# Optimization experiments

Hardware: AMD Instinct MI355X
Metric: run time of the kernel (lower is better)

The kernel has to match this reference:

```python
import jax, jax.numpy as jnp
import numpy as np

K = 3        # kernel size (square)
PAD = 1
STRIDE = 1


def conv2d(x, w, b, stride=STRIDE, pad=PAD):
    out = jax.lax.conv_general_dilated(
        x, w, (stride, stride), [(pad, pad), (pad, pad)],
        dimension_numbers=('NCHW', 'OIHW', 'NCHW'))
    return out + b[None, :, None, None]


def deform_sample(x, offset, mask):
    """Bilinear sampling at learned offsets (torchvision deform_conv2d v2 semantics).
    x: (B,C,H,W); offset: (B,2*K*K,Ho,Wo) as (dy,dx) pairs per kernel tap;
    mask: (B,K*K,Ho,Wo) already sigmoided. Returns (B,C,K*K,Ho,Wo)."""
    B, C, H, W = x.shape
    KK = mask.shape[1]
    Ho, Wo = offset.shape[2], offset.shape[3]
    off = offset.reshape(B, KK, 2, Ho, Wo)
    dy, dx = off[:, :, 0], off[:, :, 1]                      # (B,KK,Ho,Wo)
    ky, kx = jnp.meshgrid(jnp.arange(K), jnp.arange(K), indexing='ij')
    ky = ky.reshape(-1).astype(x.dtype)                       # (KK,)
    kx = kx.reshape(-1).astype(x.dtype)
    base_y = (jnp.arange(Ho) * STRIDE - PAD).astype(x.dtype)  # (Ho,)
    base_x = (jnp.arange(Wo) * STRIDE - PAD).astype(x.dtype)
    py = base_y[None, None, :, None] + ky[None, :, None, None] + dy
    px = base_x[None, None, None, :] + kx[None, :, None, None] + dx
    y0 = jnp.floor(py)
    x0 = jnp.floor(px)
    wy1 = py - y0; wx1 = px - x0
    wy0 = 1.0 - wy1; wx0 = 1.0 - wx1

    def gather(yi, xi):
        # zero-padded bilinear corner gather -> (B,C,KK,Ho,Wo)
        valid = ((yi >= 0) & (yi < H) & (xi >= 0) & (xi < W)).astype(x.dtype)
        yc = jnp.clip(yi, 0, H - 1).astype(jnp.int32)
        xc = jnp.clip(xi, 0, W - 1).astype(jnp.int32)
        vals = jax.vmap(lambda xb, yb, xib: xb[:, yb, xib])(x, yc, xc)
        return vals * valid[:, None]

    samp = (gather(y0, x0) * (wy0 * wx0)[:, None]
            + gather(y0, x0 + 1.0) * (wy0 * wx1)[:, None]
            + gather(y0 + 1.0, x0) * (wy1 * wx0)[:, None]
            + gather(y0 + 1.0, x0 + 1.0) * (wy1 * wx1)[:, None])
    return samp * mask[:, None]


def setup_inputs() -> dict:
    key = jax.random.key(0)
    k = jax.random.split(key, 8)
    B, Cin, Cout, H, W = 4, 256, 256, 64, 64
    stdv = 1.0 / np.sqrt(Cin * K * K)
    x = jax.random.normal(k[0], (B, Cin, H, W), dtype=jnp.float32)
    weight = jax.random.uniform(k[1], (Cout, Cin, K, K), minval=-stdv, maxval=stdv, dtype=jnp.float32)
    bias = jnp.zeros((Cout,), dtype=jnp.float32)
    # offset/mask convs are zero-init in the original; use small random values
    # so the irregular-sampling path is actually exercised.
    off_w = jax.random.normal(k[2], (2 * K * K, Cin, K, K), dtype=jnp.float32) * 0.01
    off_b = jax.random.normal(k[3], (2 * K * K,), dtype=jnp.float32) * 0.5
    mask_w = jax.random.normal(k[4], (K * K, Cin, K, K), dtype=jnp.float32) * 0.01
    mask_b = jax.random.normal(k[5], (K * K,), dtype=jnp.float32) * 0.1
    return {"x": x, "weight": weight, "bias": bias,
            "off_w": off_w, "off_b": off_b, "mask_w": mask_w, "mask_b": mask_b}


def reference(x, weight, bias, off_w, off_b, mask_w, mask_b):
    offset = conv2d(x, off_w, off_b)                      # (B,2*KK,H,W)
    mask = jax.nn.sigmoid(conv2d(x, mask_w, mask_b))      # (B,KK,H,W)
    samp = deform_sample(x, offset, mask)                 # (B,C,KK,H,W)
    O, C = weight.shape[0], weight.shape[1]
    out = jnp.einsum('bckhw,ock->bohw', samp, weight.reshape(O, C, K * K))
    return out + bias[None, :, None, None]
```

## Files before the change

### kernel.cpp

```cpp
#include <hip/hip_runtime.h>
#include <hip/hip_bf16.h>
#include <string.h>


typedef __attribute__((ext_vector_type(8))) short short8;
typedef __attribute__((ext_vector_type(8))) _Float16 half8;
typedef __attribute__((ext_vector_type(2))) _Float16 half2v;
typedef __attribute__((ext_vector_type(16))) float floatx16;

__device__ __forceinline__ unsigned bfbits(float f) {
    unsigned u;
    __builtin_memcpy(&u, &f, 4);
    return (u + 0x7fffu + ((u >> 16) & 1u)) >> 16;
}
__device__ __forceinline__ unsigned pack_bf16(float lo, float hi) {
    return bfbits(lo) | (bfbits(hi) << 16);
}
__device__ __forceinline__ unsigned pack_f16(float lo, float hi) {
    _Float16 a = (_Float16)lo, b = (_Float16)hi;
    unsigned short ua, ub;
    __builtin_memcpy(&ua, &a, 2);
    __builtin_memcpy(&ub, &b, 2);
    return (unsigned)ua | ((unsigned)ub << 16);
}

__device__ __forceinline__ void gl_lds16(const void* g, void* l) {
    __builtin_amdgcn_global_load_lds(
        (const __attribute__((address_space(1))) unsigned int*)g,
        (__attribute__((address_space(3))) unsigned int*)l,
        16, 0, 0);
}

__global__ __launch_bounds__(256) void xpose_hwc_kernel(
    const float* __restrict__ x, unsigned short* __restrict__ xt)
{
    __shared__ float stage[256 * 65];
    const int bid = blockIdx.x;
    const int b = bid >> 6, y = bid & 63;
    const int tid = threadIdx.x;
    const float* src = x + (size_t)b * 256 * 4096 + y * 64;

#pragma unroll
    for (int i = 0; i < 16; ++i) {
        int idx = i * 256 + tid;
        int c = idx >> 4, xq = idx & 15;
        float4 v = *(const float4*)&src[(size_t)c * 4096 + xq * 4];
        stage[c * 65 + xq * 4 + 0] = v.x;
        stage[c * 65 + xq * 4 + 1] = v.y;
        stage[c * 65 + xq * 4 + 2] = v.z;
        stage[c * 65 + xq * 4 + 3] = v.w;
    }
    __syncthreads();

    unsigned short* dst = xt + (size_t)bid * 16384;
#pragma unroll
    for (int i = 0; i < 32; ++i) {
        int c2 = (tid & 127) * 2;
        int xx = i * 2 + (tid >> 7);
        float f0 = stage[c2 * 65 + xx];
        float f1 = stage[(c2 + 1) * 65 + xx];
        *(unsigned*)&dst[xx * 256 + c2] = pack_f16(f0, f1);
    }
}

__global__ __launch_bounds__(256) void weight_pack_kernel(
    const float* __restrict__ w, const float* __restrict__ off_w,
    const float* __restrict__ mask_w,
    unsigned short* __restrict__ ws_b, unsigned short* __restrict__ ws_a2)
{
    __shared__ float slab[32 * 289];
    const int bid = blockIdx.x;
    const int tid = threadIdx.x;

    if (bid < 64) {
        const int nt = bid >> 3, cb = bid & 7;
        const float* wbase = w + (size_t)nt * 32 * 2304 + cb * 288;
#pragma unroll
        for (int i = 0; i < 9; ++i) {
            int idx = i * 256 + tid;
            int o = idx / 72, f4 = idx % 72;
            float4 v = *(const float4*)&wbase[(size_t)o * 2304 + f4 * 4];
            slab[o * 289 + f4 * 4 + 0] = v.x;
            slab[o * 289 + f4 * 4 + 1] = v.y;
            slab[o * 289 + f4 * 4 + 2] = v.z;
            slab[o * 289 + f4 * 4 + 3] = v.w;
        }
        __syncthreads();
#pragma unroll
        for (int pass = 0; pass < 5; ++pass) {
            int rid = pass * 8 + (tid >> 5);
            if (rid < 36) {
                int kk = rid >> 2, q = rid & 3;
                int no = tid & 31;
                unsigned pk[4];
#pragma unroll
                for (int i = 0; i < 4; ++i) {
                    float f0 = slab[no * 289 + (q * 8 + 2 * i) * 9 + kk];
                    float f1 = slab[no * 289 + (q * 8 + 2 * i + 1) * 9 + kk];
                    pk[i] = pack_f16(f0, f1);
                }
                size_t u = ((size_t)nt * 288 + kk * 32 + cb * 4 + q) * 32 + no;
                *(uint4*)&ws_b[u * 8] = make_uint4(pk[0], pk[1], pk[2], pk[3]);
            }
        }
    } else {
        int e = (bid - 64) * 256 + tid;
        int lan = e & 31;
        int ku = e >> 5;
        int kk = ku >> 5;
        int c0 = (ku & 31) * 8;
        int o = lan;
        float f[8];
#pragma unroll
        for (int j = 0; j < 8; ++j) {
            int c = c0 + j;
            float v = 0.f;
            if (o < 18)      v = off_w[((size_t)o * 256 + c) * 9 + kk];
            else if (o < 27) v = mask_w[((size_t)(o - 18) * 256 + c) * 9 + kk];
            f[j] = v;
        }
        unsigned pk[4];
#pragma unroll
        for (int i = 0; i < 4; ++i) pk[i] = pack_f16(f[2 * i], f[2 * i + 1]);
        *(uint4*)&ws_a2[(size_t)e * 8] = make_uint4(pk[0], pk[1], pk[2], pk[3]);
    }
}

__global__ __launch_bounds__(512) void offmask_mfma_kernel(
    const unsigned short* __restrict__ xt, const unsigned short* __restrict__ ws_a2,
    const float* __restrict__ off_b, const float* __restrict__ mask_b,
    float* __restrict__ ws_off)
{
    __shared__ uint4 stage[3 * 66 * 32];
    const int bid = blockIdx.x;
    const int row = (bid & 7) * 32 + (bid >> 3);
    const int b = row >> 6, ho = row & 63;
    const int tid = threadIdx.x;
    const int l = tid & 63;
    const int w = tid >> 6;
    const int lan = l & 31, h = l >> 5;
    const int ntile = w >> 2, kq = w & 3;

    const char* xtb = (const char*)xt + (size_t)b * 64 * 32768;
    for (int r = 0; r < 3; ++r) {
        int y = ho - 1 + r;
        uint4* rowbase = &stage[r * 66 * 32];
        if (y >= 0 && y < 64) {
            const char* src = xtb + (size_t)y * 32768;
#pragma unroll
            for (int i = 0; i < 4; ++i) {
                int g0 = 32 + (w * 4 + i) * 64;
                int g = g0 + l;
                int p01 = g >> 5, j = g & 31;
                int kul = j ^ (p01 & 7);
                gl_lds16(src + ((size_t)(p01 - 1) * 32 + kul) * 16,
                         rowbase + g0);
            }
            if (tid < 64) {
                int g = (tid < 32) ? tid : (2080 + (tid - 32));
                rowbase[g] = make_uint4(0, 0, 0, 0);
            }
        } else {
            for (int g = tid; g < 2112; g += 512)
                rowbase[g] = make_uint4(0, 0, 0, 0);
        }
    }
    __syncthreads();

    floatx16 acc;
#pragma unroll
    for (int r = 0; r < 16; ++r) acc[r] = 0.f;

    const uint4* a4 = (const uint4*)ws_a2;
    const int n = ntile * 32 + lan;
#pragma unroll
    for (int ky = 0; ky < 3; ++ky) {
#pragma unroll
        for (int kx = 0; kx < 3; ++kx) {
            int kk = ky * 3 + kx;
            int p01 = n + kx;
#pragma unroll
            for (int s4 = 0; s4 < 4; ++s4) {
                int s = kq * 4 + s4;
                int kul = s * 2 + h;
                uint4 ua = a4[(size_t)(kk * 32 + kul) * 32 + lan];
                uint4 ub = stage[(ky * 66 + p01) * 32 + (kul ^ (p01 & 7))];
                half8 a, bb;
                __builtin_memcpy(&a, &ua, 16);
                __builtin_memcpy(&bb, &ub, 16);
                acc = __builtin_amdgcn_mfma_f32_32x32x16_f16(a, bb, acc, 0, 0, 0);
            }
        }
    }
    __syncthreads();

    float* red = (float*)stage;
#pragma unroll
    for (int r = 0; r < 16; ++r) red[(w * 64 + l) * 16 + r] = acc[r];
    __syncthreads();
    for (int idx = tid; idx < 27 * 64; idx += 512) {
        int oc = idx >> 6, wo = idx & 63;
        int nt2 = wo >> 5, nn = wo & 31;
        int h2 = (oc >> 2) & 1;
        int r = (oc & 3) | ((oc >> 3) << 2);
        int lane2 = nn + 32 * h2;
        float s = 0.f;
#pragma unroll
        for (int kq2 = 0; kq2 < 4; ++kq2)
            s += red[((nt2 * 4 + kq2) * 64 + lane2) * 16 + r];
        float v;
        if (oc < 18) {
            v = s + off_b[oc];
        } else {
            float t = s + mask_b[oc - 18];
            v = 1.f / (1.f + expf(-t));
        }
        ws_off[(size_t)row * 1728 + idx] = v;
    }
}

__global__ __launch_bounds__(512, 2) void deform_gemm_kernel(
    const unsigned short* __restrict__ xt, const float* __restrict__ ws_off,
    const unsigned short* __restrict__ ws_b, const float* __restrict__ bias,
    float* __restrict__ out)
{
    __shared__ uint4 paramw[576];
    __shared__ ushort4 paramo[576];
    __shared__ float biasl[256];
    __shared__ uint4 tile[2][2048];

    const int bid = blockIdx.x;
    const int row = (bid & 7) * 32 + (bid >> 3);
    const int b = row >> 6, ho = row & 63;
    const int tid = threadIdx.x;
    const int l = tid & 63;
    const int wid = tid >> 6;
    const int lan = l & 31;
    const int h = l >> 5;

    if (tid < 256) biasl[tid] = bias[tid];

    {
        const float* ob = ws_off + (size_t)row * 1728;
        for (int it = tid; it < 576; it += 512) {
            int kk = it >> 6, p = it & 63;
            float dy = ob[(2 * kk) * 64 + p];
            float dx = ob[(2 * kk + 1) * 64 + p];
            float mk = ob[(18 + kk) * 64 + p];
            int ky = kk / 3, kx = kk - ky * 3;
            float py = (float)(ho - 1 + ky) + dy;
            float px = (float)(p - 1 + kx) + dx;
            float y0f = floorf(py), x0f = floorf(px);
            float wy1 = py - y0f, wx1 = px - x0f;
            float wy0 = 1.f - wy1, wx0 = 1.f - wx1;
            int y0 = (int)y0f, xi0 = (int)x0f;
            int y1 = y0 + 1, xi1 = xi0 + 1;
            float vy0 = (y0 >= 0 && y0 < 64) ? 1.f : 0.f;
            float vy1 = (y1 >= 0 && y1 < 64) ? 1.f : 0.f;
            float vx0 = (xi0 >= 0 && xi0 < 64) ? 1.f : 0.f;
            float vx1 = (xi1 >= 0 && xi1 < 64) ? 1.f : 0.f;
            float wr0 = wy0 * vy0 * mk, wr1 = wy1 * vy1 * mk;
            float wa = wx0 * vx0, wb2 = wx1 * vx1;
            int yc0 = min(max(y0, 0), 63), yc1 = min(max(y1, 0), 63);
            int xc0 = min(max(xi0, 0), 63), xc1 = min(max(xi1, 0), 63);
            float a00 = wr0 * wa, a01 = wr0 * wb2;
            float a10 = wr1 * wa, a11 = wr1 * wb2;
            paramw[it] = make_uint4(pack_f16(a00, a00), pack_f16(a01, a01),
                                    pack_f16(a10, a10), pack_f16(a11, a11));
            paramo[it] = make_ushort4((unsigned short)(yc0 * 64 + xc0),
                                      (unsigned short)(yc0 * 64 + xc1),
                                      (unsigned short)(yc1 * 64 + xc0),
                                      (unsigned short)(yc1 * 64 + xc1));
        }
    }
    __syncthreads();

    const char* xb16 = (const char*)xt + ((size_t)b << 21);
    const uint4* wb4 = (const uint4*)ws_b;

    floatx16 acc0, acc1;
#pragma unroll
    for (int r = 0; r < 16; ++r) { acc0[r] = 0.f; acc1[r] = 0.f; }

    uint4 gA[2][4], gB[2][4];
    uint4 wvA[2], wvB[2];
    uint4 uaA[8], uaB[8];

    auto issue_half = [&](int kk, int i0, uint4 (&g)[2][4], uint4 (&wv)[2]) {
#pragma unroll
        for (int i = 0; i < 2; ++i) {
            int p = wid * 8 + 2 * (i0 + i) + h;
            int e = kk * 64 + p;
            wv[i] = paramw[e];
            ushort4 uo = paramo[e];
            __builtin_memcpy(&g[i][0], xb16 + ((int)uo.x << 9) + (lan << 4), 16);
            __builtin_memcpy(&g[i][1], xb16 + ((int)uo.y << 9) + (lan << 4), 16);
            __builtin_memcpy(&g[i][2], xb16 + ((int)uo.z << 9) + (lan << 4), 16);
            __builtin_memcpy(&g[i][3], xb16 + ((int)uo.w << 9) + (lan << 4), 16);
        }
    };

    auto pack_half = [&](int buf, int i0, uint4 (&g)[2][4], uint4 (&wv)[2]) {
        char* tb = (char*)&tile[buf][0];
#pragma unroll
        for (int i = 0; i < 2; ++i) {
            int p = wid * 8 + 2 * (i0 + i) + h;
            half2v c00[4], c01[4], c10[4], c11[4], w00, w01, w10, w11;
            __builtin_memcpy(&c00, &g[i][0], 16);
            __builtin_memcpy(&c01, &g[i][1], 16);
            __builtin_memcpy(&c10, &g[i][2], 16);
            __builtin_memcpy(&c11, &g[i][3], 16);
            __builtin_memcpy(&w00, &wv[i].x, 4);
            __builtin_memcpy(&w01, &wv[i].y, 4);
            __builtin_memcpy(&w10, &wv[i].z, 4);
            __builtin_memcpy(&w11, &wv[i].w, 4);
            uint4 outv;
            unsigned* op = (unsigned*)&outv;
#pragma unroll
            for (int j = 0; j < 4; ++j) {
                half2v r = c00[j] * w00;
                r = c01[j] * w01 + r;
                r = c10[j] * w10 + r;
                r = c11[j] * w11 + r;
                __builtin_memcpy(&op[j], &r, 4);
            }
            __builtin_memcpy(tb + lan * 1024 + ((p << 4) ^ (lan << 4)), &outv, 16);
        }
    };

    issue_half(0, 0, gA, wvA);
    pack_half(0, 0, gA, wvA);
    issue_half(0, 2, gB, wvB);
    pack_half(0, 2, gB, wvB);
#pragma unroll
    for (int ks = 0; ks < 8; ++ks) {
        int kul = ks * 2 + h;
        uaA[ks] = wb4[((size_t)wid * 288 + 0 * 32 + kul) * 32 + lan];
    }
    __syncthreads();

    for (int kk = 0; kk < 9; ++kk) {
        const int buf = kk & 1, nbuf = (kk + 1) & 1;

#pragma unroll
        for (int ks = 0; ks < 8; ++ks) {
            int kul = (ks + 8) * 2 + h;
            uaB[ks] = wb4[((size_t)wid * 288 + kk * 32 + kul) * 32 + lan];
        }
        if (kk < 8) issue_half(kk + 1, 0, gA, wvA);
        __builtin_amdgcn_sched_barrier(0);

        {
            const char* tb = (const char*)&tile[buf][0];
#pragma unroll
            for (int ks = 0; ks < 8; ++ks) {
                int kul = ks * 2 + h;
                uint4 ub0, ub1;
                __builtin_memcpy(&ub0, tb + kul * 1024 + ((lan << 4) ^ (kul << 4)), 16);
                __builtin_memcpy(&ub1, tb + kul * 1024 + (((32 + lan) << 4) ^ (kul << 4)), 16);
                half8 a, b0, b1;
                __builtin_memcpy(&a, &uaA[ks], 16);
                __builtin_memcpy(&b0, &ub0, 16);
                __builtin_memcpy(&b1, &ub1, 16);
                acc0 = __builtin_amdgcn_mfma_f32_32x32x16_f16(a, b0, acc0, 0, 0, 0);
                acc1 = __builtin_amdgcn_mfma_f32_32x32x16_f16(a, b1, acc1, 0, 0, 0);
            }
        }
        __builtin_amdgcn_sched_barrier(0);

        if (kk < 8) {
#pragma unroll
            for (int ks = 0; ks < 8; ++ks) {
                int kul = ks * 2 + h;
                uaA[ks] = wb4[((size_t)wid * 288 + (kk + 1) * 32 + kul) * 32 + lan];
            }
            pack_half(nbuf, 0, gA, wvA);
            issue_half(kk + 1, 2, gB, wvB);
        }
        __builtin_amdgcn_sched_barrier(0);

        {
            const char* tb = (const char*)&tile[buf][0];
#pragma unroll
            for (int ks = 0; ks < 8; ++ks) {
                int kul = (ks + 8) * 2 + h;
                uint4 ub0, ub1;
                __builtin_memcpy(&ub0, tb + kul * 1024 + ((lan << 4) ^ (kul << 4)), 16);
                __builtin_memcpy(&ub1, tb + kul * 1024 + (((32 + lan) << 4) ^ (kul << 4)), 16);
                half8 a, b0, b1;
                __builtin_memcpy(&a, &uaB[ks], 16);
                __builtin_memcpy(&b0, &ub0, 16);
                __builtin_memcpy(&b1, &ub1, 16);
                acc0 = __builtin_amdgcn_mfma_f32_32x32x16_f16(a, b0, acc0, 0, 0, 0);
                acc1 = __builtin_amdgcn_mfma_f32_32x32x16_f16(a, b1, acc1, 0, 0, 0);
            }
        }
        __builtin_amdgcn_sched_barrier(0);

        if (kk < 8) pack_half(nbuf, 2, gB, wvB);
        __syncthreads();
    }

#pragma unroll
    for (int nt = 0; nt < 2; ++nt) {
#pragma unroll
        for (int r = 0; r < 16; ++r) {
            int o = wid * 32 + (r & 3) + 8 * (r >> 2) + 4 * h;
            int woo = nt * 32 + lan;
            float v = (nt == 0) ? acc0[r] : acc1[r];
            out[(((size_t)b * 256 + o) * 64 + ho) * 64 + woo] = v + biasl[o];
        }
    }
}

extern "C" void kernel_launch(void* const* d_in, const int* in_sizes, int n_in,
                              void* d_out, int out_size, void* d_ws, size_t ws_size,
                              hipStream_t stream) {
    const float* x      = (const float*)d_in[0];
    const float* weight = (const float*)d_in[1];
    const float* bias   = (const float*)d_in[2];
    const float* off_w  = (const float*)d_in[3];
    const float* off_b  = (const float*)d_in[4];
    const float* mask_w = (const float*)d_in[5];
    const float* mask_b = (const float*)d_in[6];
    float* out = (float*)d_out;

    float* ws_off = (float*)d_ws;
    unsigned short* ws_b  = (unsigned short*)((char*)d_ws + 1769472);
    unsigned short* ws_a2 = (unsigned short*)((char*)d_ws + 2949120);
    unsigned short* xt    = (unsigned short*)((char*)d_ws + 3096576);

    hipLaunchKernelGGL(weight_pack_kernel, dim3(100), dim3(256), 0, stream,
                       weight, off_w, mask_w, ws_b, ws_a2);
    hipLaunchKernelGGL(xpose_hwc_kernel, dim3(256), dim3(256), 0, stream,
                       x, xt);
    hipLaunchKernelGGL(offmask_mfma_kernel, dim3(256), dim3(512), 0, stream,
                       xt, ws_a2, off_b, mask_b, ws_off);
    hipLaunchKernelGGL(deform_gemm_kernel, dim3(256), dim3(512), 0, stream,
                       xt, ws_off, ws_b, bias, out);
}
```

Before: 124.0 us.

## Fuse offset/mask conv into deformable GEMM kernel via shared LDS

Merges the offset/mask MFMA convolution kernel into the deformable sampling GEMM kernel. Each block computes its row's offsets and mask into shared memory and then runs the sampling GEMM, reusing one LDS buffer for the staging, reduction and tile regions. This removes one kernel launch and the global round-trip of the offset workspace. In exchange the fused kernel needs a large static LDS allocation (about 100KB plus extras), which may limit occupancy to one block per CU despite the launch bound of 2, and it serializes the two phases within each block.

```diff
diff --git a/kernel.cpp b/kernel.cpp
--- a/kernel.cpp
+++ b/kernel.cpp
@@ -126,108 +126,16 @@
     }
 }
 
-__global__ __launch_bounds__(512) void offmask_mfma_kernel(
-    const unsigned short* __restrict__ xt, const unsigned short* __restrict__ ws_a2,
+__global__ __launch_bounds__(512, 2) void fused_deform_kernel(
+    const unsigned short* __restrict__ xt,
+    const unsigned short* __restrict__ ws_a2,
+    const unsigned short* __restrict__ ws_b,
     const float* __restrict__ off_b, const float* __restrict__ mask_b,
-    float* __restrict__ ws_off)
+    const float* __restrict__ bias, float* __restrict__ out)
 {
-    __shared__ uint4 stage[3 * 66 * 32];
-    const int bid = blockIdx.x;
-    const int row = (bid & 7) * 32 + (bid >> 3);
-    const int b = row >> 6, ho = row & 63;
-    const int tid = threadIdx.x;
-    const int l = tid & 63;
-    const int w = tid >> 6;
-    const int lan = l & 31, h = l >> 5;
-    const int ntile = w >> 2, kq = w & 3;
-
-    const char* xtb = (const char*)xt + (size_t)b * 64 * 32768;
-    for (int r = 0; r < 3; ++r) {
-        int y = ho - 1 + r;
-        uint4* rowbase = &stage[r * 66 * 32];
-        if (y >= 0 && y < 64) {
-            const char* src = xtb + (size_t)y * 32768;
-#pragma unroll
-            for (int i = 0; i < 4; ++i) {
-                int g0 = 32 + (w * 4 + i) * 64;
-                int g = g0 + l;
-                int p01 = g >> 5, j = g & 31;
-                int kul = j ^ (p01 & 7);
-                gl_lds16(src + ((size_t)(p01 - 1) * 32 + kul) * 16,
-                         rowbase + g0);
-            }
-            if (tid < 64) {
-                int g = (tid < 32) ? tid : (2080 + (tid - 32));
-                rowbase[g] = make_uint4(0, 0, 0, 0);
-            }
-        } else {
-            for (int g = tid; g < 2112; g += 512)
-                rowbase[g] = make_uint4(0, 0, 0, 0);
-        }
-    }
-    __syncthreads();
-
-    floatx16 acc;
-#pragma unroll
-    for (int r = 0; r < 16; ++r) acc[r] = 0.f;
-
-    const uint4* a4 = (const uint4*)ws_a2;
-    const int n = ntile * 32 + lan;
-#pragma unroll
-    for (int ky = 0; ky < 3; ++ky) {
-#pragma unroll
-        for (int kx = 0; kx < 3; ++kx) {
-            int kk = ky * 3 + kx;
-            int p01 = n + kx;
-#pragma unroll
-            for (int s4 = 0; s4 < 4; ++s4) {
-                int s = kq * 4 + s4;
-                int kul = s * 2 + h;
-                uint4 ua = a4[(size_t)(kk * 32 + kul) * 32 + lan];
-                uint4 ub = stage[(ky * 66 + p01) * 32 + (kul ^ (p01 & 7))];
-                half8 a, bb;
-                __builtin_memcpy(&a, &ua, 16);
-                __builtin_memcpy(&bb, &ub, 16);
-                acc = __builtin_amdgcn_mfma_f32_32x32x16_f16(a, bb, acc, 0, 0, 0);
-            }
-        }
-    }
-    __syncthreads();
-
-    float* red = (float*)stage;
-#pragma unroll
-    for (int r = 0; r < 16; ++r) red[(w * 64 + l) * 16 + r] = acc[r];
-    __syncthreads();
-    for (int idx = tid; idx < 27 * 64; idx += 512) {
-        int oc = idx >> 6, wo = idx & 63;
-        int nt2 = wo >> 5, nn = wo & 31;
-        int h2 = (oc >> 2) & 1;
-        int r = (oc & 3) | ((oc >> 3) << 2);
-        int lane2 = nn + 32 * h2;
-        float s = 0.f;
-#pragma unroll
-        for (int kq2 = 0; kq2 < 4; ++kq2)
-            s += red[((nt2 * 4 + kq2) * 64 + lane2) * 16 + r];
-        float v;
-        if (oc < 18) {
-            v = s + off_b[oc];
-        } else {
-            float t = s + mask_b[oc - 18];
-            v = 1.f / (1.f + expf(-t));
-        }
-        ws_off[(size_t)row * 1728 + idx] = v;
-    }
-}
-
-__global__ __launch_bounds__(512, 2) void deform_gemm_kernel(
-    const unsigned short* __restrict__ xt, const float* __restrict__ ws_off,
-    const unsigned short* __restrict__ ws_b, const float* __restrict__ bias,
-    float* __restrict__ out)
-{
-    __shared__ uint4 paramw[576];
-    __shared__ ushort4 paramo[576];
+    __shared__ __align__(16) char smem[101376];
+    __shared__ float offrow[1728];
     __shared__ float biasl[256];
-    __shared__ uint4 tile[2][2048];
 
     const int bid = blockIdx.x;
     const int row = (bid & 7) * 32 + (bid >> 3);
@@ -235,18 +143,100 @@
     const int tid = threadIdx.x;
     const int l = tid & 63;
     const int wid = tid >> 6;
-    const int lan = l & 31;
-    const int h = l >> 5;
+    const int lan = l & 31, h = l >> 5;
 
     if (tid < 256) biasl[tid] = bias[tid];
 
     {
-        const float* ob = ws_off + (size_t)row * 1728;
+        uint4* stage = (uint4*)smem;
+        const int ntile = wid >> 2, kq = wid & 3;
+        const char* xtb = (const char*)xt + (size_t)b * 64 * 32768;
+        for (int r = 0; r < 3; ++r) {
+            int y = ho - 1 + r;
+            uint4* rowbase = &stage[r * 66 * 32];
+            if (y >= 0 && y < 64) {
+                const char* src = xtb + (size_t)y * 32768;
+#pragma unroll
+                for (int i = 0; i < 4; ++i) {
+                    int g0 = 32 + (wid * 4 + i) * 64;
+                    int g = g0 + l;
+                    int p01 = g >> 5, j = g & 31;
+                    int kul = j ^ (p01 & 7);
+                    gl_lds16(src + ((size_t)(p01 - 1) * 32 + kul) * 16,
+                             rowbase + g0);
+                }
+                if (tid < 64) {
+                    int g = (tid < 32) ? tid : (2080 + (tid - 32));
+                    rowbase[g] = make_uint4(0, 0, 0, 0);
+                }
+            } else {
+                for (int g = tid; g < 2112; g += 512)
+                    rowbase[g] = make_uint4(0, 0, 0, 0);
+            }
+        }
+        __syncthreads();
+
+        floatx16 acc;
+#pragma unroll
+        for (int r = 0; r < 16; ++r) acc[r] = 0.f;
+
+        const uint4* a4 = (const uint4*)ws_a2;
+        const int n = ntile * 32 + lan;
+#pragma unroll
+        for (int ky = 0; ky < 3; ++ky) {
+#pragma unroll
+            for (int kx = 0; kx < 3; ++kx) {
+                int kk = ky * 3 + kx;
+                int p01 = n + kx;
+#pragma unroll
+                for (int s4 = 0; s4 < 4; ++s4) {
+                    int s = kq * 4 + s4;
+                    int kul = s * 2 + h;
+                    uint4 ua = a4[(size_t)(kk * 32 + kul) * 32 + lan];
+                    uint4 ub = stage[(ky * 66 + p01) * 32 + (kul ^ (p01 & 7))];
+                    half8 a, bb;
+                    __builtin_memcpy(&a, &ua, 16);
+                    __builtin_memcpy(&bb, &ub, 16);
+                    acc = __builtin_amdgcn_mfma_f32_32x32x16_f16(a, bb, acc, 0, 0, 0);
+                }
+            }
+        }
+        __syncthreads();
+
+        float* red = (float*)smem;
+#pragma unroll
+        for (int r = 0; r < 16; ++r) red[(wid * 64 + l) * 16 + r] = acc[r];
+        __syncthreads();
+        for (int idx = tid; idx < 27 * 64; idx += 512) {
+            int oc = idx >> 6, wo = idx & 63;
+            int nt2 = wo >> 5, nn = wo & 31;
+            int h2 = (oc >> 2) & 1;
+            int r = (oc & 3) | ((oc >> 3) << 2);
+            int lane2 = nn + 32 * h2;
+            float s = 0.f;
+#pragma unroll
+            for (int kq2 = 0; kq2 < 4; ++kq2)
+                s += red[((nt2 * 4 + kq2) * 64 + lane2) * 16 + r];
+            float v;
+            if (oc < 18) {
+                v = s + off_b[oc];
+            } else {
+                float t = s + mask_b[oc - 18];
+                v = 1.f / (1.f + expf(-t));
+            }
+            offrow[idx] = v;
+        }
+    }
+    __syncthreads();
+
+    uint4*   paramw = (uint4*)(smem + 65536);
+    ushort4* paramo = (ushort4*)(smem + 65536 + 9216);
+    {
         for (int it = tid; it < 576; it += 512) {
             int kk = it >> 6, p = it & 63;
-            float dy = ob[(2 * kk) * 64 + p];
-            float dx = ob[(2 * kk + 1) * 64 + p];
-            float mk = ob[(18 + kk) * 64 + p];
+            float dy = offrow[(2 * kk) * 64 + p];
+            float dx = offrow[(2 * kk + 1) * 64 + p];
+            float mk = offrow[(18 + kk) * 64 + p];
             int ky = kk / 3, kx = kk - ky * 3;
             float py = (float)(ho - 1 + ky) + dy;
             float px = (float)(p - 1 + kx) + dx;
@@ -301,7 +291,7 @@
     };
 
     auto pack_half = [&](int buf, int i0, uint4 (&g)[2][4], uint4 (&wv)[2]) {
-        char* tb = (char*)&tile[buf][0];
+        char* tb = smem + buf * 32768;
 #pragma unroll
         for (int i = 0; i < 2; ++i) {
             int p = wid * 8 + 2 * (i0 + i) + h;
@@ -351,7 +341,7 @@
         __builtin_amdgcn_sched_barrier(0);
 
         {
-            const char* tb = (const char*)&tile[buf][0];
+            const char* tb = smem + buf * 32768;
 #pragma unroll
             for (int ks = 0; ks < 8; ++ks) {
                 int kul = ks * 2 + h;
@@ -380,7 +370,7 @@
         __builtin_amdgcn_sched_barrier(0);
 
         {
-            const char* tb = (const char*)&tile[buf][0];
+            const char* tb = smem + buf * 32768;
 #pragma unroll
             for (int ks = 0; ks < 8; ++ks) {
                 int kul = (ks + 8) * 2 + h;
@@ -425,17 +415,14 @@
     const float* mask_b = (const float*)d_in[6];
     float* out = (float*)d_out;
 
-    float* ws_off = (float*)d_ws;
-    unsigned short* ws_b  = (unsigned short*)((char*)d_ws + 1769472);
-    unsigned short* ws_a2 = (unsigned short*)((char*)d_ws + 2949120);
-    unsigned short* xt    = (unsigned short*)((char*)d_ws + 3096576);
+    unsigned short* ws_b  = (unsigned short*)d_ws;
+    unsigned short* ws_a2 = (unsigned short*)((char*)d_ws + 1179648);
+    unsigned short* xt    = (unsigned short*)((char*)d_ws + 1327104);
 
     hipLaunchKernelGGL(weight_pack_kernel, dim3(100), dim3(256), 0, stream,
                        weight, off_w, mask_w, ws_b, ws_a2);
     hipLaunchKernelGGL(xpose_hwc_kernel, dim3(256), dim3(256), 0, stream,
                        x, xt);
-    hipLaunchKernelGGL(offmask_mfma_kernel, dim3(256), dim3(512), 0, stream,
-                       xt, ws_a2, off_b, mask_b, ws_off);
-    hipLaunchKernelGGL(deform_gemm_kernel, dim3(256), dim3(512), 0, stream,
-                       xt, ws_off, ws_b, bias, out);
-}
+    hipLaunchKernelGGL(fused_deform_kernel, dim3(256), dim3(512), 0, stream,
+                       xt, ws_a2, ws_b, off_b, mask_b, bias, out);
+}
```

New measurement: 123.2 us. Within noise of the previous version (-0.7%).
